# Kernel optimization log

Measured on AMD Instinct MI355X. Metric: run time of the kernel, lower is better.

## Reference

```python
import jax, jax.numpy as jnp
import numpy as np

N = 50000    # nodes
E = 640000   # edges (avg degree ~12.8)
IN_NF = 64   # raw atom features
D = 96       # hidden dim
H = 4 * D    # 384
L = 4        # RPETConv layers
G = 512      # graphs in the batch
NOUT = 2


def setup_inputs():
    key = jax.random.key(0)
    ks = iter(jax.random.split(key, 64))
    def lin(shape):
        fi = shape[-2]
        return jax.random.normal(next(ks), shape, jnp.float32) / np.float32(np.sqrt(fi))
    inp = {}
    inp['x'] = jax.random.normal(next(ks), (N, IN_NF), jnp.float32)
    inp['edge_attr'] = jax.random.normal(next(ks), (E, D), jnp.float32)
    inp['emb_W1'] = lin((IN_NF, H)); inp['emb_b1'] = jnp.zeros((H,), jnp.float32)
    inp['emb_W2'] = lin((H, D));     inp['emb_b2'] = jnp.zeros((D,), jnp.float32)
    for nm in ('Wq', 'Wk', 'Wv', 'ffn_W1', 'ffn_W2'):
        inp[nm] = lin((L, D, D))
    for nm in ('bq', 'bk', 'bv', 'ffn_b1', 'ffn_b2', 'n1_b', 'n2_b'):
        inp[nm] = jnp.zeros((L, D), jnp.float32)
    inp['n1_g'] = jnp.ones((L, D), jnp.float32)
    inp['n2_g'] = jnp.ones((L, D), jnp.float32)
    inp['u_W1'] = lin((D, H)); inp['u_b1'] = jnp.zeros((H,), jnp.float32)
    inp['u_W2'] = lin((H, H)); inp['u_b2'] = jnp.zeros((H,), jnp.float32)
    inp['u_g'] = jnp.ones((H,), jnp.float32); inp['u_b'] = jnp.zeros((H,), jnp.float32)
    inp['clf_W'] = lin((H, NOUT)); inp['clf_b'] = jnp.zeros((NOUT,), jnp.float32)
    inp['rec_W1'] = lin((H, H)); inp['rec_b1'] = jnp.zeros((H,), jnp.float32)
    inp['rec_W2'] = lin((H, IN_NF)); inp['rec_b2'] = jnp.zeros((IN_NF,), jnp.float32)
    inp['edge_index'] = jax.random.randint(next(ks), (2, E), 0, N, jnp.int32)
    inp['batch_index'] = jnp.sort(jax.random.randint(next(ks), (N,), 0, G, jnp.int32))
    return inp


def _ln(x, g, b):
    # torch.nn.LayerNorm, eps=1e-5
    m = x.mean(-1, keepdims=True)
    v = ((x - m) ** 2).mean(-1, keepdims=True)
    return (x - m) * jax.lax.rsqrt(v + 1e-5) * g + b


def _forward(fs, edge_index, batch_index):
    (x, edge_attr, emb_W1, emb_b1, emb_W2, emb_b2,
     Wq, bq, Wk, bk, Wv, bv, n1_g, n1_b,
     ffn_W1, ffn_b1, ffn_W2, ffn_b2, n2_g, n2_b,
     u_W1, u_b1, u_W2, u_b2, u_g, u_b,
     clf_W, clf_b, rec_W1, rec_b1, rec_W2, rec_b2) = fs
    src, dst = edge_index[0], edge_index[1]  # PyG: x_j = x[src], x_i = x[dst]
    scale = D ** -0.5
    # atom embedding MLP
    h = jax.nn.relu(x @ emb_W1 + emb_b1) @ emb_W2 + emb_b2  # [N, D]
    for l in range(L):
        x_i = h[dst]                  # [E, D] target gather
        px = h[src] + edge_attr       # [E, D] source + relative positional edge attr
        q = x_i @ Wq[l] + bq[l]
        k = px @ Wk[l] + bk[l]
        v = px @ Wv[l] + bv[l]
        ae = jnp.exp((q * k).sum(-1) * scale)  # [E] (original uses raw exp, no max-sub)
        # faithful quirk: softmax denominator segmented over SOURCE index
        s = ae / jax.ops.segment_sum(ae, src, num_segments=N)[src]
        # aggregation (aggr='add') goes to TARGET index
        agg = jax.ops.segment_sum(s[:, None] * v, dst, num_segments=N)  # [N, D]
        h1 = _ln(h + agg, n1_g[l], n1_b[l])
        f = jax.nn.elu(h1 @ ffn_W1[l] + ffn_b1[l]) @ ffn_W2[l] + ffn_b2[l]
        h = _ln(f + h1, n2_g[l], n2_b[l])
    # updim
    u = jax.nn.leaky_relu(h @ u_W1 + u_b1, 0.01) @ u_W2 + u_b2
    u = _ln(u, u_g, u_b)              # [N, H]
    # mean readout per graph
    cnt = jnp.maximum(jax.ops.segment_sum(jnp.ones((N,), u.dtype), batch_index, num_segments=G), 1.0)
    pooled = jax.ops.segment_sum(u, batch_index, num_segments=G) / cnt[:, None]  # [G, H]
    out = pooled @ clf_W + clf_b      # [G, NOUT]
    r = jax.nn.relu(u @ rec_W1 + rec_b1) @ rec_W2 + rec_b2  # [N, IN_NF]
    return (out, r)


def reference(x, edge_attr, emb_W1, emb_b1, emb_W2, emb_b2, Wq, bq, Wk, bk, Wv, bv, n1_g, n1_b, ffn_W1, ffn_b1, ffn_W2, ffn_b2, n2_g, n2_b, u_W1, u_b1, u_W2, u_b2, u_g, u_b, clf_W, clf_b, rec_W1, rec_b1, rec_W2, rec_b2, edge_index, batch_index):
    fs = (x, edge_attr, emb_W1, emb_b1, emb_W2, emb_b2, Wq, bq, Wk, bk, Wv, bv, n1_g, n1_b,
          ffn_W1, ffn_b1, ffn_W2, ffn_b2, n2_g, n2_b, u_W1, u_b1, u_W2, u_b2, u_g, u_b,
          clf_W, clf_b, rec_W1, rec_b1, rec_W2, rec_b2)
    return _forward(fs, edge_index, batch_index)
```

## Files before the change

### kernel.cpp

```cpp
#include <hip/hip_runtime.h>
#include <math.h>

#define N_NODES 50000
#define N_EDGES 640000
#define INF_ 64
#define DD 96
#define HH 384
#define NLAYERS 4
#define NGRAPH 512
#define NOUT_ 2
#define MAXDEG 64

#define ACT_NONE 0
#define ACT_RELU 1
#define ACT_ELU 2
#define ACT_LEAKY 3

typedef unsigned int uint;
typedef unsigned short ushort;
typedef __attribute__((ext_vector_type(8))) short v8s;
typedef __attribute__((ext_vector_type(4))) float v4f;

__device__ __forceinline__ float bf_lo(uint u) { return __uint_as_float(u << 16); }
__device__ __forceinline__ float bf_hi(uint u) { return __uint_as_float(u & 0xffff0000u); }
__device__ __forceinline__ float bfs(ushort s) { return __uint_as_float(((uint)s) << 16); }
__device__ __forceinline__ ushort f2bf(float f)
{
    uint u = __float_as_uint(f);
    return (ushort)((u + 0x7fffu + ((u >> 16) & 1u)) >> 16);
}

template<int BN, int ACT, bool ACCUM, bool OUT16>
__global__ __launch_bounds__(256)
void gemm_mf(const ushort* __restrict__ A, const ushort* __restrict__ Bt,
             const float* __restrict__ bias, float* __restrict__ C32,
             ushort* __restrict__ C16, int M, int Nc, int K)
{
    const int BM = 128, LDA = 40;
    const int FN = BN / 32;
    __shared__ ushort As[BM * LDA];
    __shared__ ushort Bs[BN * LDA];
    int tid = threadIdx.x;
    int lane = tid & 63, wave = tid >> 6;
    int ln15 = lane & 15, quad = lane >> 4;
    int wm = (wave >> 1) * 64, wn = (wave & 1) * (BN / 2);
    int bm0 = blockIdx.x * BM, bn0 = blockIdx.y * BN;

    v4f acc[4][FN];
    #pragma unroll
    for (int i = 0; i < 4; i++)
        #pragma unroll
        for (int j = 0; j < FN; j++) acc[i][j] = (v4f){0.f, 0.f, 0.f, 0.f};

    for (int k0 = 0; k0 < K; k0 += 32) {
        #pragma unroll
        for (int it = 0; it < 2; it++) {
            int u = it * 256 + tid;
            int r = u >> 2, c8 = (u & 3) * 8;
            int row = bm0 + r;
            int4 v = make_int4(0, 0, 0, 0);
            if (row < M) v = *(const int4*)&A[(size_t)row * K + k0 + c8];
            *(int4*)&As[r * LDA + c8] = v;
        }
        #pragma unroll
        for (int it = 0; it < (BN * 4 + 255) / 256; it++) {
            int u = it * 256 + tid;
            if ((BN * 4) % 256 == 0 || u < BN * 4) {
                int r = u >> 2, c8 = (u & 3) * 8;
                *(int4*)&Bs[r * LDA + c8] =
                    *(const int4*)&Bt[(size_t)(bn0 + r) * K + k0 + c8];
            }
        }
        __syncthreads();
        v8s af[4], bf[FN];
        #pragma unroll
        for (int i = 0; i < 4; i++)
            af[i] = *(const v8s*)&As[(wm + i * 16 + ln15) * LDA + quad * 8];
        #pragma unroll
        for (int j = 0; j < FN; j++)
            bf[j] = *(const v8s*)&Bs[(wn + j * 16 + ln15) * LDA + quad * 8];
        #pragma unroll
        for (int i = 0; i < 4; i++)
            #pragma unroll
            for (int j = 0; j < FN; j++)
                acc[i][j] = __builtin_amdgcn_mfma_f32_16x16x32_bf16(
                    af[i], bf[j], acc[i][j], 0, 0, 0);
        __syncthreads();
    }
    #pragma unroll
    for (int i = 0; i < 4; i++) {
        #pragma unroll
        for (int j = 0; j < FN; j++) {
            int col = bn0 + wn + j * 16 + ln15;
            float bsv = bias ? bias[col] : 0.f;
            #pragma unroll
            for (int r = 0; r < 4; r++) {
                int row = bm0 + wm + i * 16 + quad * 4 + r;
                if (row >= M) continue;
                float v = acc[i][j][r] + bsv;
                if (ACCUM) v += C32[(size_t)row * Nc + col];
                if (ACT == ACT_RELU)       v = fmaxf(v, 0.f);
                else if (ACT == ACT_ELU)   v = v > 0.f ? v : expm1f(v);
                else if (ACT == ACT_LEAKY) v = v > 0.f ? v : 0.01f * v;
                if (OUT16) C16[(size_t)row * Nc + col] = f2bf(v);
                else       C32[(size_t)row * Nc + col] = v;
            }
        }
    }
}

__device__ __forceinline__ float wave_reduce_sum(float v)
{
    #pragma unroll
    for (int o = 32; o > 0; o >>= 1) v += __shfl_xor(v, o, 64);
    return v;
}

__global__ __launch_bounds__(256)
void cvt16(const float* __restrict__ in, ushort* __restrict__ out, long n)
{
    long i = ((long)blockIdx.x * 256 + threadIdx.x) * 4;
    if (i >= n) return;
    float4 v = *(const float4*)&in[i];
    ushort4 o;
    o.x = f2bf(v.x); o.y = f2bf(v.y); o.z = f2bf(v.z); o.w = f2bf(v.w);
    *(ushort4*)&out[i] = o;
}

__global__ __launch_bounds__(256)
void wqk_k(const float* __restrict__ Wq, const float* __restrict__ Wk,
           const float* __restrict__ bq, float* __restrict__ Wcat, float* __restrict__ bcat)
{
    int l = blockIdx.y;
    int idx = blockIdx.x * 256 + threadIdx.x;
    const float* wq = Wq + (size_t)l * DD * DD;
    const float* wk = Wk + (size_t)l * DD * DD;
    if (idx < DD * DD) {
        int k = idx / DD, j = idx % DD;
        float s = 0.f;
        for (int t = 0; t < DD; t++) s += wq[k * DD + t] * wk[j * DD + t];
        Wcat[(size_t)l * DD * 4 * DD + (size_t)k * 4 * DD + 288 + j] = s;
    }
    if (idx < DD) {
        int j = idx;
        float s = 0.f;
        for (int t = 0; t < DD; t++) s += bq[l * DD + t] * wk[j * DD + t];
        bcat[l * 4 * DD + 288 + j] = s;
    }
}

__global__ __launch_bounds__(256)
void pack_k(const float* __restrict__ Wq, const float* __restrict__ Wk,
            const float* __restrict__ Wv, const float* __restrict__ bq,
            const float* __restrict__ bk, const float* __restrict__ bv,
            float* __restrict__ Wcat, float* __restrict__ bcat)
{
    int idx = blockIdx.x * 256 + threadIdx.x;
    if (idx >= NLAYERS * DD * 288) return;
    int l = idx / (DD * 288);
    int rem = idx % (DD * 288);
    int k = rem / 288, n = rem % 288;
    int which = n / DD, j = n % DD;
    const float* W = which == 0 ? Wq : (which == 1 ? Wk : Wv);
    Wcat[(size_t)l * DD * 4 * DD + (size_t)k * 4 * DD + n] =
        W[(size_t)l * DD * DD + k * DD + j];
    if (k == 0) {
        const float* bb = which == 0 ? bq : (which == 1 ? bk : bv);
        bcat[l * 4 * DD + n] = bb[l * DD + j];
    }
}

#define NPACK 22
struct PackArgs {
    const float* src[NPACK];
    ushort* dst[NPACK];
    int K[NPACK], N[NPACK];
};
__global__ __launch_bounds__(256)
void packT_k(PackArgs pa)
{
    int w = blockIdx.y;
    int K = pa.K[w], N = pa.N[w];
    int idx = blockIdx.x * 256 + threadIdx.x;
    if (idx >= K * N) return;
    int n = idx / K, k = idx % K;
    pa.dst[w][(size_t)n * K + k] = f2bf(pa.src[w][(size_t)k * N + n]);
}

__global__ __launch_bounds__(256)
void scatter_k(const int* __restrict__ src, const int* __restrict__ dst,
               int* __restrict__ deg, int2* __restrict__ pe)
{
    int e = blockIdx.x * 256 + threadIdx.x;
    if (e >= N_EDGES) return;
    int d = dst[e];
    int c = atomicAdd(&deg[d], 1);
    if (c < MAXDEG) pe[(size_t)d * MAXDEG + c] = make_int2(src[e], e);
}

template<bool EA16>
__global__ __launch_bounds__(256)
void edge1w(const ushort* __restrict__ qkv16, const void* __restrict__ eaP,
            const int2* __restrict__ pe, const int* __restrict__ deg,
            float* __restrict__ ae_slot, float* __restrict__ denom, float scale)
{
    int lane = threadIdx.x & 63;
    int half = lane >> 5, l32 = lane & 31;
    int d = blockIdx.x * 4 + (threadIdx.x >> 6);
    if (d >= N_NODES) return;
    int cnt = deg[d]; if (cnt > MAXDEG) cnt = MAXDEG;
    if (cnt == 0) return;
    const uint* qrow = (const uint*)(qkv16 + (size_t)d * 384);
    const uint* prow = (const uint*)(qkv16 + (size_t)d * 384 + 288);
    uint qu0 = qrow[l32], pu0 = prow[l32];
    uint qu1 = 0, pu1 = 0;
    if (l32 < 16) { qu1 = qrow[32 + l32]; pu1 = prow[32 + l32]; }
    float q00 = bf_lo(qu0), q01 = bf_hi(qu0), q10 = bf_lo(qu1), q11 = bf_hi(qu1);
    float p00 = bf_lo(pu0), p01 = bf_hi(pu0), p10 = bf_lo(pu1), p11 = bf_hi(pu1);
    int2 pr = pe[(size_t)d * MAXDEG + lane];
    for (int cb = 0; cb < cnt; cb += 4) {
        float dots[2];
        int sxu[2];
        #pragma unroll
        for (int u = 0; u < 2; u++) {
            int myc = cb + 2 * u + half;
            int cc = myc < cnt ? myc : cnt - 1;
            int sx = __shfl(pr.x, cc);
            int ex = __shfl(pr.y, cc);
            sxu[u] = sx;
            const uint* krow = (const uint*)(qkv16 + (size_t)sx * 384 + 96);
            uint ku0 = krow[l32];
            float e00, e01, e10 = 0.f, e11 = 0.f;
            uint ku1 = 0;
            if (EA16) {
                const uint* er = (const uint*)eaP + (size_t)ex * 48;
                uint eu0 = er[l32]; e00 = bf_lo(eu0); e01 = bf_hi(eu0);
                if (l32 < 16) {
                    uint eu1 = er[32 + l32]; e10 = bf_lo(eu1); e11 = bf_hi(eu1);
                    ku1 = krow[32 + l32];
                }
            } else {
                const float* er = (const float*)eaP + (size_t)ex * DD;
                float2 ef0 = *(const float2*)&er[2 * l32]; e00 = ef0.x; e01 = ef0.y;
                if (l32 < 16) {
                    float2 ef1 = *(const float2*)&er[64 + 2 * l32]; e10 = ef1.x; e11 = ef1.y;
                    ku1 = krow[32 + l32];
                }
            }
            float dot = q00 * bf_lo(ku0) + q01 * bf_hi(ku0)
                      + p00 * e00 + p01 * e01 + p10 * e10 + p11 * e11;
            if (l32 < 16) dot += q10 * bf_lo(ku1) + q11 * bf_hi(ku1);
            dots[u] = dot;
        }
        #pragma unroll
        for (int o = 16; o > 0; o >>= 1) {
            dots[0] += __shfl_xor(dots[0], o);
            dots[1] += __shfl_xor(dots[1], o);
        }
        #pragma unroll
        for (int u = 0; u < 2; u++) {
            int myc = cb + 2 * u + half;
            if (l32 == 0 && myc < cnt) {
                float v = __expf(dots[u] * scale);
                ae_slot[(size_t)d * MAXDEG + myc] = v;
                atomicAdd(&denom[sxu[u]], v);
            }
        }
    }
}

template<bool EA16>
__global__ __launch_bounds__(256)
void edge2w(const ushort* __restrict__ qkv16, const void* __restrict__ eaP,
            const float* __restrict__ ae_slot, const float* __restrict__ denom,
            const int2* __restrict__ pe, const int* __restrict__ deg,
            float* __restrict__ agg, ushort* __restrict__ T16)
{
    int lane = threadIdx.x & 63;
    int half = lane >> 5, l32 = lane & 31;
    int d = blockIdx.x * 4 + (threadIdx.x >> 6);
    if (d >= N_NODES) return;
    int cnt = deg[d]; if (cnt > MAXDEG) cnt = MAXDEG;
    int2 pr = pe[(size_t)d * MAXDEG + lane];
    float ar = ae_slot[(size_t)d * MAXDEG + lane];
    float a00 = 0.f, a01 = 0.f, a10 = 0.f, a11 = 0.f;
    float t00 = 0.f, t01 = 0.f, t10 = 0.f, t11 = 0.f;
    for (int cb = 0; cb < cnt; cb += 4) {
        #pragma unroll
        for (int u = 0; u < 2; u++) {
            int myc = cb + 2 * u + half;
            int cc = myc < cnt ? myc : cnt - 1;
            int sx = __shfl(pr.x, cc);
            int ex = __shfl(pr.y, cc);
            float ae = __shfl(ar, cc);
            float w = (myc < cnt) ? ae / denom[sx] : 0.f;
            const uint* vrow = (const uint*)(qkv16 + (size_t)sx * 384 + 192);
            uint vu0 = vrow[l32];
            float e00, e01, e10 = 0.f, e11 = 0.f;
            uint vu1 = 0;
            if (EA16) {
                const uint* er = (const uint*)eaP + (size_t)ex * 48;
                uint eu0 = er[l32]; e00 = bf_lo(eu0); e01 = bf_hi(eu0);
                if (l32 < 16) {
                    uint eu1 = er[32 + l32]; e10 = bf_lo(eu1); e11 = bf_hi(eu1);
                    vu1 = vrow[32 + l32];
                }
            } else {
                const float* er = (const float*)eaP + (size_t)ex * DD;
                float2 ef0 = *(const float2*)&er[2 * l32]; e00 = ef0.x; e01 = ef0.y;
                if (l32 < 16) {
                    float2 ef1 = *(const float2*)&er[64 + 2 * l32]; e10 = ef1.x; e11 = ef1.y;
                    vu1 = vrow[32 + l32];
                }
            }
            a00 += w * bf_lo(vu0); a01 += w * bf_hi(vu0);
            t00 += w * e00; t01 += w * e01;
            if (l32 < 16) {
                a10 += w * bf_lo(vu1); a11 += w * bf_hi(vu1);
                t10 += w * e10; t11 += w * e11;
            }
        }
    }
    a00 += __shfl_xor(a00, 32); a01 += __shfl_xor(a01, 32);
    a10 += __shfl_xor(a10, 32); a11 += __shfl_xor(a11, 32);
    t00 += __shfl_xor(t00, 32); t01 += __shfl_xor(t01, 32);
    t10 += __shfl_xor(t10, 32); t11 += __shfl_xor(t11, 32);
    if (half == 0) {
        *(float2*)&agg[(size_t)d * DD + 2 * l32] = make_float2(a00, a01);
        ((uint*)T16)[(size_t)d * 48 + l32] = ((uint)f2bf(t01) << 16) | f2bf(t00);
        if (l32 < 16) {
            *(float2*)&agg[(size_t)d * DD + 64 + 2 * l32] = make_float2(a10, a11);
            ((uint*)T16)[(size_t)d * 48 + 32 + l32] = ((uint)f2bf(t11) << 16) | f2bf(t10);
        }
    }
}

template<int RL, int BMODE>
__global__ __launch_bounds__(256)
void ln_b(const ushort* __restrict__ a, const void* __restrict__ bP,
          const float* __restrict__ g, const float* __restrict__ beta,
          ushort* __restrict__ out, int M)
{
    int wave = threadIdx.x >> 6;
    int lane = threadIdx.x & 63;
    int row = blockIdx.x * 4 + wave;
    if (row >= M) return;
    const int NE = (RL + 63) / 64;
    float vals[NE];
    float s = 0.f;
    #pragma unroll
    for (int i = 0; i < NE; i++) {
        int j = lane + i * 64;
        float x = 0.f;
        if (j < RL) {
            x = bfs(a[(size_t)row * RL + j]);
            if (BMODE == 1) x += ((const float*)bP)[(size_t)row * RL + j];
            if (BMODE == 2) x += bfs(((const ushort*)bP)[(size_t)row * RL + j]);
        }
        vals[i] = x; s += x;
    }
    s = wave_reduce_sum(s);
    float mean = s / RL;
    float sq = 0.f;
    #pragma unroll
    for (int i = 0; i < NE; i++) {
        int j = lane + i * 64;
        if (j < RL) { float dd = vals[i] - mean; sq += dd * dd; }
    }
    sq = wave_reduce_sum(sq);
    float rstd = rsqrtf(sq / RL + 1e-5f);
    #pragma unroll
    for (int i = 0; i < NE; i++) {
        int j = lane + i * 64;
        if (j < RL)
            out[(size_t)row * RL + j] = f2bf((vals[i] - mean) * rstd * g[j] + beta[j]);
    }
}

#define PCHUNK 64
__global__ __launch_bounds__(192)
void pool2_k(const ushort* __restrict__ u, const int* __restrict__ batch,
             float* __restrict__ pooled, float* __restrict__ cnt)
{
    int j = threadIdx.x;
    int n0 = blockIdx.x * PCHUNK;
    if (n0 >= N_NODES) return;
    int n1 = n0 + PCHUNK; if (n1 > N_NODES) n1 = N_NODES;
    float a0 = 0.f, a1 = 0.f;
    int cur = batch[n0];
    int runStart = n0;
    for (int n = n0; n < n1; n++) {
        int bg = batch[n];
        if (bg != cur) {
            atomicAdd(&pooled[(size_t)cur * HH + 2 * j], a0);
            atomicAdd(&pooled[(size_t)cur * HH + 2 * j + 1], a1);
            if (j == 0) atomicAdd(&cnt[cur], (float)(n - runStart));
            a0 = 0.f; a1 = 0.f; cur = bg; runStart = n;
        }
        uint v = ((const uint*)u)[(size_t)n * 192 + j];
        a0 += bf_lo(v); a1 += bf_hi(v);
    }
    atomicAdd(&pooled[(size_t)cur * HH + 2 * j], a0);
    atomicAdd(&pooled[(size_t)cur * HH + 2 * j + 1], a1);
    if (j == 0) atomicAdd(&cnt[cur], (float)(n1 - runStart));
}

__global__ __launch_bounds__(64)
void clf_k(const float* __restrict__ pooled, const float* __restrict__ cnt,
           const float* __restrict__ W, const float* __restrict__ bcl,
           float* __restrict__ out)
{
    int g = blockIdx.x;
    int lane = threadIdx.x;
    float c = cnt[g]; c = c > 1.f ? c : 1.f;
    float inv = 1.f / c;
    float a0 = 0.f, a1 = 0.f;
    #pragma unroll
    for (int i = 0; i < 6; i++) {
        int j = lane + i * 64;
        float pv = pooled[(size_t)g * HH + j] * inv;
        a0 += pv * W[j * 2 + 0];
        a1 += pv * W[j * 2 + 1];
    }
    a0 = wave_reduce_sum(a0);
    a1 = wave_reduce_sum(a1);
    if (lane == 0) {
        out[g * 2 + 0] = a0 + bcl[0];
        out[g * 2 + 1] = a1 + bcl[1];
    }
}

extern "C" void kernel_launch(void* const* d_in, const int* in_sizes, int n_in,
                              void* d_out, int out_size, void* d_ws, size_t ws_size,
                              hipStream_t stream)
{
    const float* x       = (const float*)d_in[0];
    const float* ea      = (const float*)d_in[1];
    const float* emb_W1  = (const float*)d_in[2];
    const float* emb_b1  = (const float*)d_in[3];
    const float* emb_W2  = (const float*)d_in[4];
    const float* emb_b2  = (const float*)d_in[5];
    const float* Wq      = (const float*)d_in[6];
    const float* Wk      = (const float*)d_in[7];
    const float* Wv      = (const float*)d_in[8];
    const float* ffn_W1  = (const float*)d_in[9];
    const float* ffn_W2  = (const float*)d_in[10];
    const float* bq      = (const float*)d_in[11];
    const float* bk      = (const float*)d_in[12];
    const float* bv      = (const float*)d_in[13];
    const float* ffn_b1  = (const float*)d_in[14];
    const float* ffn_b2  = (const float*)d_in[15];
    const float* n1_b    = (const float*)d_in[16];
    const float* n2_b    = (const float*)d_in[17];
    const float* n1_g    = (const float*)d_in[18];
    const float* n2_g    = (const float*)d_in[19];
    const float* u_W1    = (const float*)d_in[20];
    const float* u_b1    = (const float*)d_in[21];
    const float* u_W2    = (const float*)d_in[22];
    const float* u_b2    = (const float*)d_in[23];
    const float* u_g     = (const float*)d_in[24];
    const float* u_bb    = (const float*)d_in[25];
    const float* clf_W   = (const float*)d_in[26];
    const float* clf_b   = (const float*)d_in[27];
    const float* rec_W1  = (const float*)d_in[28];
    const float* rec_b1  = (const float*)d_in[29];
    const float* rec_W2  = (const float*)d_in[30];
    const float* rec_b2  = (const float*)d_in[31];
    const int* edge_index = (const int*)d_in[32];
    const int* batch     = (const int*)d_in[33];
    const int* srcI = edge_index;
    const int* dstI = edge_index + N_EDGES;

    float* out   = (float*)d_out;
    float* r_out = out + NGRAPH * NOUT_;

    char* base = (char*)d_ws;
    size_t off = 0;
    auto alloc = [&](size_t bytes) -> char* {
        char* r = base + off;
        off += (bytes + 255) & ~(size_t)255;
        return r;
    };
    ushort* h16     = (ushort*)alloc((size_t)N_NODES * DD * 2);
    ushort* qkv16   = (ushort*)alloc((size_t)N_NODES * HH * 2);
    float*  agg     = (float*) alloc((size_t)N_NODES * DD * 4);
    ushort* T16     = (ushort*)alloc((size_t)N_NODES * DD * 2);
    ushort* h116    = (ushort*)alloc((size_t)N_NODES * DD * 2);
    int2*   pe      = (int2*)  alloc((size_t)N_NODES * MAXDEG * 8);
    float*  ae_slot = (float*) alloc((size_t)N_NODES * MAXDEG * 4);
    ushort* f116    = (ushort*)alloc((size_t)N_NODES * DD * 2);
    float*  denom   = (float*) alloc((size_t)N_NODES * 4);
    int*    deg     = (int*)   alloc((size_t)N_NODES * 4);
    float*  pooled  = (float*) alloc((size_t)NGRAPH * HH * 4);
    float*  cnt     = (float*) alloc(NGRAPH * 4);
    float*  Wcat    = (float*) alloc((size_t)NLAYERS * DD * 4 * DD * 4);
    float*  bcat    = (float*) alloc((size_t)NLAYERS * 4 * DD * 4);
    ushort* x16     = (ushort*)alloc((size_t)N_NODES * INF_ * 2);
    ushort* embW1T  = (ushort*)alloc((size_t)HH * INF_ * 2);
    ushort* embW2T  = (ushort*)alloc((size_t)DD * HH * 2);
    ushort* WcatT   = (ushort*)alloc((size_t)NLAYERS * HH * DD * 2);
    ushort* WvT     = (ushort*)alloc((size_t)NLAYERS * DD * DD * 2);
    ushort* fW1T    = (ushort*)alloc((size_t)NLAYERS * DD * DD * 2);
    ushort* fW2T    = (ushort*)alloc((size_t)NLAYERS * DD * DD * 2);
    ushort* uW1T    = (ushort*)alloc((size_t)HH * DD * 2);
    ushort* uW2T    = (ushort*)alloc((size_t)HH * HH * 2);
    ushort* recW1T  = (ushort*)alloc((size_t)HH * HH * 2);
    ushort* recW2T  = (ushort*)alloc((size_t)INF_ * HH * 2);
    ushort* ea16 = (ushort*)alloc((size_t)N_EDGES * DD * 2);
    bool use_ea16 = (ws_size >= off);
    const void* eaP = use_ea16 ? (const void*)ea16 : (const void*)ea;

    ushort* t16    = qkv16;
    ushort* upre16 = (ushort*)agg;
    ushort* u16    = (ushort*)pe;
    ushort* rtmp16 = qkv16;

    dim3 blk(256);
    const int GB = (N_NODES + 127) / 128;
    const float scale = 1.f / sqrtf((float)DD);

    wqk_k<<<dim3(36, NLAYERS), blk, 0, stream>>>(Wq, Wk, bq, Wcat, bcat);
    pack_k<<<(NLAYERS * DD * 288 + 255) / 256, blk, 0, stream>>>(
        Wq, Wk, Wv, bq, bk, bv, Wcat, bcat);
    PackArgs pa;
    int pi = 0;
    auto addp = [&](const float* s, ushort* d, int K, int N) {
        pa.src[pi] = s; pa.dst[pi] = d; pa.K[pi] = K; pa.N[pi] = N; pi++;
    };
    addp(emb_W1, embW1T, INF_, HH);
    addp(emb_W2, embW2T, HH, DD);
    for (int l = 0; l < NLAYERS; l++) addp(Wcat + (size_t)l * DD * 4 * DD, WcatT + (size_t)l * HH * DD, DD, HH);
    for (int l = 0; l < NLAYERS; l++) addp(Wv + (size_t)l * DD * DD, WvT + (size_t)l * DD * DD, DD, DD);
    for (int l = 0; l < NLAYERS; l++) addp(ffn_W1 + (size_t)l * DD * DD, fW1T + (size_t)l * DD * DD, DD, DD);
    for (int l = 0; l < NLAYERS; l++) addp(ffn_W2 + (size_t)l * DD * DD, fW2T + (size_t)l * DD * DD, DD, DD);
    addp(u_W1, uW1T, DD, HH);
    addp(u_W2, uW2T, HH, HH);
    addp(rec_W1, recW1T, HH, HH);
    addp(rec_W2, recW2T, HH, INF_);
    packT_k<<<dim3(576, NPACK), blk, 0, stream>>>(pa);

    cvt16<<<((size_t)N_NODES * INF_ / 4 + 255) / 256, blk, 0, stream>>>(
        x, x16, (long)N_NODES * INF_);
    if (use_ea16)
        cvt16<<<((size_t)N_EDGES * DD / 4 + 255) / 256, blk, 0, stream>>>(
            ea, ea16, (long)N_EDGES * DD);

    gemm_mf<128, ACT_RELU, false, true><<<dim3(GB, 3), blk, 0, stream>>>(
        x16, embW1T, emb_b1, nullptr, t16, N_NODES, HH, INF_);
    gemm_mf<96, ACT_NONE, false, true><<<dim3(GB, 1), blk, 0, stream>>>(
        t16, embW2T, emb_b2, nullptr, h16, N_NODES, DD, HH);

    hipMemsetAsync(deg, 0, N_NODES * sizeof(int), stream);
    scatter_k<<<(N_EDGES + 255) / 256, blk, 0, stream>>>(srcI, dstI, deg, pe);

    const int EGRID = (N_NODES + 3) / 4;
    for (int l = 0; l < NLAYERS; l++) {
        gemm_mf<128, ACT_NONE, false, true><<<dim3(GB, 3), blk, 0, stream>>>(
            h16, WcatT + (size_t)l * HH * DD, bcat + (size_t)l * 4 * DD,
            nullptr, qkv16, N_NODES, HH, DD);

        hipMemsetAsync(denom, 0, N_NODES * sizeof(float), stream);
        if (use_ea16) {
            edge1w<true><<<EGRID, blk, 0, stream>>>(
                qkv16, eaP, pe, deg, ae_slot, denom, scale);
            edge2w<true><<<EGRID, blk, 0, stream>>>(
                qkv16, eaP, ae_slot, denom, pe, deg, agg, T16);
        } else {
            edge1w<false><<<EGRID, blk, 0, stream>>>(
                qkv16, eaP, pe, deg, ae_slot, denom, scale);
            edge2w<false><<<EGRID, blk, 0, stream>>>(
                qkv16, eaP, ae_slot, denom, pe, deg, agg, T16);
        }

        gemm_mf<96, ACT_NONE, true, false><<<dim3(GB, 1), blk, 0, stream>>>(
            T16, WvT + (size_t)l * DD * DD, nullptr, agg, nullptr, N_NODES, DD, DD);

        ln_b<DD, 1><<<(N_NODES + 3) / 4, blk, 0, stream>>>(
            h16, agg, n1_g + (size_t)l * DD, n1_b + (size_t)l * DD, h116, N_NODES);

        gemm_mf<96, ACT_ELU, false, true><<<dim3(GB, 1), blk, 0, stream>>>(
            h116, fW1T + (size_t)l * DD * DD, ffn_b1 + (size_t)l * DD,
            nullptr, f116, N_NODES, DD, DD);
        gemm_mf<96, ACT_NONE, false, true><<<dim3(GB, 1), blk, 0, stream>>>(
            f116, fW2T + (size_t)l * DD * DD, ffn_b2 + (size_t)l * DD,
            nullptr, T16, N_NODES, DD, DD);
        ln_b<DD, 2><<<(N_NODES + 3) / 4, blk, 0, stream>>>(
            T16, h116, n2_g + (size_t)l * DD, n2_b + (size_t)l * DD, h16, N_NODES);
    }

    gemm_mf<128, ACT_LEAKY, false, true><<<dim3(GB, 3), blk, 0, stream>>>(
        h16, uW1T, u_b1, nullptr, t16, N_NODES, HH, DD);
    gemm_mf<128, ACT_NONE, false, true><<<dim3(GB, 3), blk, 0, stream>>>(
        t16, uW2T, u_b2, nullptr, upre16, N_NODES, HH, HH);
    ln_b<HH, 0><<<(N_NODES + 3) / 4, blk, 0, stream>>>(
        upre16, nullptr, u_g, u_bb, u16, N_NODES);

    hipMemsetAsync(pooled, 0, (size_t)(NGRAPH * HH + NGRAPH) * sizeof(float), stream);
    pool2_k<<<(N_NODES + PCHUNK - 1) / PCHUNK, 192, 0, stream>>>(u16, batch, pooled, cnt);
    clf_k<<<NGRAPH, 64, 0, stream>>>(pooled, cnt, clf_W, clf_b, out);

    gemm_mf<128, ACT_RELU, false, true><<<dim3(GB, 3), blk, 0, stream>>>(
        u16, recW1T, rec_b1, nullptr, rtmp16, N_NODES, HH, HH);
    gemm_mf<64, ACT_NONE, false, false><<<dim3(GB, 1), blk, 0, stream>>>(
        rtmp16, recW2T, rec_b2, r_out, nullptr, N_NODES, INF_, HH);
}
```

Before: 1.662 ms.

## Fuse GEMM with residual LayerNorm and regroup edge kernels into 16-lane groups

```diff
diff --git a/kernel.cpp b/kernel.cpp
--- a/kernel.cpp
+++ b/kernel.cpp
@@ -109,6 +109,138 @@
     }
 }
 
+template<bool ACC32>
+__global__ __launch_bounds__(256)
+void gemm_ln(const ushort* __restrict__ A, const ushort* __restrict__ Bt,
+             const float* __restrict__ bias, const float* __restrict__ C32,
+             const ushort* __restrict__ add16,
+             const float* __restrict__ g, const float* __restrict__ beta,
+             ushort* __restrict__ out, int M, int K)
+{
+    const int BM = 128, LDA = 40, FN = 3;
+    __shared__ ushort As[BM * LDA];
+    __shared__ ushort Bs[96 * LDA];
+    __shared__ float2 red[2][2][64];
+    int tid = threadIdx.x;
+    int lane = tid & 63, wave = tid >> 6;
+    int ln15 = lane & 15, quad = lane >> 4;
+    int wm = (wave >> 1) * 64, wn = (wave & 1) * 48;
+    int bm0 = blockIdx.x * BM;
+
+    v4f acc[4][FN];
+    #pragma unroll
+    for (int i = 0; i < 4; i++)
+        #pragma unroll
+        for (int j = 0; j < FN; j++) acc[i][j] = (v4f){0.f, 0.f, 0.f, 0.f};
+
+    for (int k0 = 0; k0 < K; k0 += 32) {
+        #pragma unroll
+        for (int it = 0; it < 2; it++) {
+            int u = it * 256 + tid;
+            int r = u >> 2, c8 = (u & 3) * 8;
+            int row = bm0 + r;
+            int4 v = make_int4(0, 0, 0, 0);
+            if (row < M) v = *(const int4*)&A[(size_t)row * K + k0 + c8];
+            *(int4*)&As[r * LDA + c8] = v;
+        }
+        #pragma unroll
+        for (int it = 0; it < 2; it++) {
+            int u = it * 256 + tid;
+            if (u < 384) {
+                int r = u >> 2, c8 = (u & 3) * 8;
+                *(int4*)&Bs[r * LDA + c8] =
+                    *(const int4*)&Bt[(size_t)r * K + k0 + c8];
+            }
+        }
+        __syncthreads();
+        v8s af[4], bf[FN];
+        #pragma unroll
+        for (int i = 0; i < 4; i++)
+            af[i] = *(const v8s*)&As[(wm + i * 16 + ln15) * LDA + quad * 8];
+        #pragma unroll
+        for (int j = 0; j < FN; j++)
+            bf[j] = *(const v8s*)&Bs[(wn + j * 16 + ln15) * LDA + quad * 8];
+        #pragma unroll
+        for (int i = 0; i < 4; i++)
+            #pragma unroll
+            for (int j = 0; j < FN; j++)
+                acc[i][j] = __builtin_amdgcn_mfma_f32_16x16x32_bf16(
+                    af[i], bf[j], acc[i][j], 0, 0, 0);
+        __syncthreads();
+    }
+
+    float s1a[4][4], s2a[4][4];
+    #pragma unroll
+    for (int i = 0; i < 4; i++)
+        #pragma unroll
+        for (int r = 0; r < 4; r++) { s1a[i][r] = 0.f; s2a[i][r] = 0.f; }
+
+    #pragma unroll
+    for (int i = 0; i < 4; i++) {
+        #pragma unroll
+        for (int j = 0; j < FN; j++) {
+            int col = wn + j * 16 + ln15;
+            float bsv = bias ? bias[col] : 0.f;
+            #pragma unroll
+            for (int r = 0; r < 4; r++) {
+                int row = bm0 + wm + i * 16 + quad * 4 + r;
+                float v = acc[i][j][r] + bsv;
+                if (row < M) {
+                    if (ACC32) v += C32[(size_t)row * DD + col];
+                    v += bfs(add16[(size_t)row * DD + col]);
+                }
+                acc[i][j][r] = v;
+                s1a[i][r] += v; s2a[i][r] += v * v;
+            }
+        }
+    }
+    #pragma unroll
+    for (int o = 1; o <= 8; o <<= 1) {
+        #pragma unroll
+        for (int i = 0; i < 4; i++)
+            #pragma unroll
+            for (int r = 0; r < 4; r++) {
+                s1a[i][r] += __shfl_xor(s1a[i][r], o);
+                s2a[i][r] += __shfl_xor(s2a[i][r], o);
+            }
+    }
+    if (ln15 == 0) {
+        #pragma unroll
+        for (int i = 0; i < 4; i++)
+            #pragma unroll
+            for (int r = 0; r < 4; r++)
+                red[wave >> 1][wave & 1][i * 16 + quad * 4 + r] =
+                    make_float2(s1a[i][r], s2a[i][r]);
+    }
+    __syncthreads();
+    float gj[FN], bj[FN];
+    #pragma unroll
+    for (int j = 0; j < FN; j++) {
+        gj[j] = g[wn + j * 16 + ln15];
+        bj[j] = beta[wn + j * 16 + ln15];
+    }
+    #pragma unroll
+    for (int i = 0; i < 4; i++) {
+        #pragma unroll
+        for (int r = 0; r < 4; r++) {
+            int row = bm0 + wm + i * 16 + quad * 4 + r;
+            if (row >= M) continue;
+            float2 o = red[wave >> 1][(wave & 1) ^ 1][i * 16 + quad * 4 + r];
+            float tot1 = s1a[i][r] + o.x;
+            float tot2 = s2a[i][r] + o.y;
+            float mean = tot1 * (1.f / 96.f);
+            float var  = tot2 * (1.f / 96.f) - mean * mean;
+            float rstd = rsqrtf(var + 1e-5f);
+            #pragma unroll
+            for (int j = 0; j < FN; j++) {
+                int col = wn + j * 16 + ln15;
+                out[(size_t)row * DD + col] =
+                    f2bf((acc[i][j][r] - mean) * rstd * gj[j] + bj[j]);
+            }
+        }
+    }
+}
+
 __device__ __forceinline__ float wave_reduce_sum(float v)
 {
     #pragma unroll
@@ -205,62 +337,61 @@
             float* __restrict__ ae_slot, float* __restrict__ denom, float scale)
 {
     int lane = threadIdx.x & 63;
-    int half = lane >> 5, l32 = lane & 31;
+    int grp = lane >> 4, t = lane & 15;
     int d = blockIdx.x * 4 + (threadIdx.x >> 6);
     if (d >= N_NODES) return;
     int cnt = deg[d]; if (cnt > MAXDEG) cnt = MAXDEG;
     if (cnt == 0) return;
-    const uint* qrow = (const uint*)(qkv16 + (size_t)d * 384);
-    const uint* prow = (const uint*)(qkv16 + (size_t)d * 384 + 288);
-    uint qu0 = qrow[l32], pu0 = prow[l32];
-    uint qu1 = 0, pu1 = 0;
-    if (l32 < 16) { qu1 = qrow[32 + l32]; pu1 = prow[32 + l32]; }
-    float q00 = bf_lo(qu0), q01 = bf_hi(qu0), q10 = bf_lo(qu1), q11 = bf_hi(qu1);
-    float p00 = bf_lo(pu0), p01 = bf_hi(pu0), p10 = bf_lo(pu1), p11 = bf_hi(pu1);
+    const uint* row = (const uint*)qkv16 + (size_t)d * 192;
+    uint qa = row[t], qb = row[16 + t], qc = row[32 + t];
+    uint pa = row[144 + t], pb = row[160 + t], pc = row[176 + t];
+    float q0l = bf_lo(qa), q0h = bf_hi(qa), q1l = bf_lo(qb), q1h = bf_hi(qb),
+          q2l = bf_lo(qc), q2h = bf_hi(qc);
+    float p0l = bf_lo(pa), p0h = bf_hi(pa), p1l = bf_lo(pb), p1h = bf_hi(pb),
+          p2l = bf_lo(pc), p2h = bf_hi(pc);
     int2 pr = pe[(size_t)d * MAXDEG + lane];
-    for (int cb = 0; cb < cnt; cb += 4) {
+    for (int cb = 0; cb < cnt; cb += 8) {
         float dots[2];
         int sxu[2];
         #pragma unroll
         for (int u = 0; u < 2; u++) {
-            int myc = cb + 2 * u + half;
+            int myc = cb + u * 4 + grp;
             int cc = myc < cnt ? myc : cnt - 1;
             int sx = __shfl(pr.x, cc);
             int ex = __shfl(pr.y, cc);
             sxu[u] = sx;
-            const uint* krow = (const uint*)(qkv16 + (size_t)sx * 384 + 96);
-            uint ku0 = krow[l32];
-            float e00, e01, e10 = 0.f, e11 = 0.f;
-            uint ku1 = 0;
+            const uint* kr = (const uint*)qkv16 + (size_t)sx * 192 + 48;
+            uint k0 = kr[t], k1 = kr[16 + t], k2 = kr[32 + t];
+            float e0l, e0h, e1l, e1h, e2l, e2h;
             if (EA16) {
                 const uint* er = (const uint*)eaP + (size_t)ex * 48;
-                uint eu0 = er[l32]; e00 = bf_lo(eu0); e01 = bf_hi(eu0);
-                if (l32 < 16) {
-                    uint eu1 = er[32 + l32]; e10 = bf_lo(eu1); e11 = bf_hi(eu1);
-                    ku1 = krow[32 + l32];
-                }
+                uint e0 = er[t], e1 = er[16 + t], e2 = er[32 + t];
+                e0l = bf_lo(e0); e0h = bf_hi(e0);
+                e1l = bf_lo(e1); e1h = bf_hi(e1);
+                e2l = bf_lo(e2); e2h = bf_hi(e2);
             } else {
                 const float* er = (const float*)eaP + (size_t)ex * DD;
-                float2 ef0 = *(const float2*)&er[2 * l32]; e00 = ef0.x; e01 = ef0.y;
-                if (l32 < 16) {
-                    float2 ef1 = *(const float2*)&er[64 + 2 * l32]; e10 = ef1.x; e11 = ef1.y;
-                    ku1 = krow[32 + l32];
-                }
-            }
-            float dot = q00 * bf_lo(ku0) + q01 * bf_hi(ku0)
-                      + p00 * e00 + p01 * e01 + p10 * e10 + p11 * e11;
-            if (l32 < 16) dot += q10 * bf_lo(ku1) + q11 * bf_hi(ku1);
-            dots[u] = dot;
-        }
-        #pragma unroll
-        for (int o = 16; o > 0; o >>= 1) {
+                float2 f0 = *(const float2*)&er[2 * t];
+                float2 f1 = *(const float2*)&er[32 + 2 * t];
+                float2 f2 = *(const float2*)&er[64 + 2 * t];
+                e0l = f0.x; e0h = f0.y; e1l = f1.x; e1h = f1.y;
+                e2l = f2.x; e2h = f2.y;
+            }
+            dots[u] = q0l * bf_lo(k0) + q0h * bf_hi(k0)
+                    + q1l * bf_lo(k1) + q1h * bf_hi(k1)
+                    + q2l * bf_lo(k2) + q2h * bf_hi(k2)
+                    + p0l * e0l + p0h * e0h + p1l * e1l + p1h * e1h
+                    + p2l * e2l + p2h * e2h;
+        }
+        #pragma unroll
+        for (int o = 8; o > 0; o >>= 1) {
             dots[0] += __shfl_xor(dots[0], o);
             dots[1] += __shfl_xor(dots[1], o);
         }
         #pragma unroll
         for (int u = 0; u < 2; u++) {
-            int myc = cb + 2 * u + half;
-            if (l32 == 0 && myc < cnt) {
+            int myc = cb + u * 4 + grp;
+            if (t == 0 && myc < cnt) {
                 float v = __expf(dots[u] * scale);
                 ae_slot[(size_t)d * MAXDEG + myc] = v;
                 atomicAdd(&denom[sxu[u]], v);
@@ -277,61 +408,65 @@
             float* __restrict__ agg, ushort* __restrict__ T16)
 {
     int lane = threadIdx.x & 63;
-    int half = lane >> 5, l32 = lane & 31;
+    int grp = lane >> 4, t = lane & 15;
     int d = blockIdx.x * 4 + (threadIdx.x >> 6);
     if (d >= N_NODES) return;
     int cnt = deg[d]; if (cnt > MAXDEG) cnt = MAXDEG;
     int2 pr = pe[(size_t)d * MAXDEG + lane];
     float ar = ae_slot[(size_t)d * MAXDEG + lane];
-    float a00 = 0.f, a01 = 0.f, a10 = 0.f, a11 = 0.f;
-    float t00 = 0.f, t01 = 0.f, t10 = 0.f, t11 = 0.f;
-    for (int cb = 0; cb < cnt; cb += 4) {
+    float a0l = 0.f, a0h = 0.f, a1l = 0.f, a1h = 0.f, a2l = 0.f, a2h = 0.f;
+    float t0l = 0.f, t0h = 0.f, t1l = 0.f, t1h = 0.f, t2l = 0.f, t2h = 0.f;
+    for (int cb = 0; cb < cnt; cb += 8) {
         #pragma unroll
         for (int u = 0; u < 2; u++) {
-            int myc = cb + 2 * u + half;
+            int myc = cb + u * 4 + grp;
             int cc = myc < cnt ? myc : cnt - 1;
             int sx = __shfl(pr.x, cc);
             int ex = __shfl(pr.y, cc);
             float ae = __shfl(ar, cc);
             float w = (myc < cnt) ? ae / denom[sx] : 0.f;
-            const uint* vrow = (const uint*)(qkv16 + (size_t)sx * 384 + 192);
-            uint vu0 = vrow[l32];
-            float e00, e01, e10 = 0.f, e11 = 0.f;
-            uint vu1 = 0;
+            const uint* vr = (const uint*)qkv16 + (size_t)sx * 192 + 96;
+            uint v0 = vr[t], v1 = vr[16 + t], v2 = vr[32 + t];
+            float e0l, e0h, e1l, e1h, e2l, e2h;
             if (EA16) {
                 const uint* er = (const uint*)eaP + (size_t)ex * 48;
-                uint eu0 = er[l32]; e00 = bf_lo(eu0); e01 = bf_hi(eu0);
-                if (l32 < 16) {
-                    uint eu1 = er[32 + l32]; e10 = bf_lo(eu1); e11 = bf_hi(eu1);
-                    vu1 = vrow[32 + l32];
-                }
+                uint e0 = er[t], e1 = er[16 + t], e2 = er[32 + t];
+                e0l = bf_lo(e0); e0h = bf_hi(e0);
+                e1l = bf_lo(e1); e1h = bf_hi(e1);
+                e2l = bf_lo(e2); e2h = bf_hi(e2);
             } else {
                 const float* er = (const float*)eaP + (size_t)ex * DD;
-                float2 ef0 = *(const float2*)&er[2 * l32]; e00 = ef0.x; e01 = ef0.y;
-                if (l32 < 16) {
-                    float2 ef1 = *(const float2*)&er[64 + 2 * l32]; e10 = ef1.x; e11 = ef1.y;
-                    vu1 = vrow[32 + l32];
-                }
-            }
-            a00 += w * bf_lo(vu0); a01 += w * bf_hi(vu0);
-            t00 += w * e00; t01 += w * e01;
-            if (l32 < 16) {
-                a10 += w * bf_lo(vu1); a11 += w * bf_hi(vu1);
-                t10 += w * e10; t11 += w * e11;
-            }
-        }
-    }
-    a00 += __shfl_xor(a00, 32); a01 += __shfl_xor(a01, 32);
-    a10 += __shfl_xor(a10, 32); a11 += __shfl_xor(a11, 32);
-    t00 += __shfl_xor(t00, 32); t01 += __shfl_xor(t01, 32);
-    t10 += __shfl_xor(t10, 32); t11 += __shfl_xor(t11, 32);
-    if (half == 0) {
-        *(float2*)&agg[(size_t)d * DD + 2 * l32] = make_float2(a00, a01);
-        ((uint*)T16)[(size_t)d * 48 + l32] = ((uint)f2bf(t01) << 16) | f2bf(t00);
-        if (l32 < 16) {
-            *(float2*)&agg[(size_t)d * DD + 64 + 2 * l32] = make_float2(a10, a11);
-            ((uint*)T16)[(size_t)d * 48 + 32 + l32] = ((uint)f2bf(t11) << 16) | f2bf(t10);
-        }
+                float2 f0 = *(const float2*)&er[2 * t];
+                float2 f1 = *(const float2*)&er[32 + 2 * t];
+                float2 f2 = *(const float2*)&er[64 + 2 * t];
+                e0l = f0.x; e0h = f0.y; e1l = f1.x; e1h = f1.y;
+                e2l = f2.x; e2h = f2.y;
+            }
+            a0l += w * bf_lo(v0); a0h += w * bf_hi(v0);
+            a1l += w * bf_lo(v1); a1h += w * bf_hi(v1);
+            a2l += w * bf_lo(v2); a2h += w * bf_hi(v2);
+            t0l += w * e0l; t0h += w * e0h;
+            t1l += w * e1l; t1h += w * e1h;
+            t2l += w * e2l; t2h += w * e2h;
+        }
+    }
+    #pragma unroll
+    for (int o = 16; o <= 32; o <<= 1) {
+        a0l += __shfl_xor(a0l, o); a0h += __shfl_xor(a0h, o);
+        a1l += __shfl_xor(a1l, o); a1h += __shfl_xor(a1h, o);
+        a2l += __shfl_xor(a2l, o); a2h += __shfl_xor(a2h, o);
+        t0l += __shfl_xor(t0l, o); t0h += __shfl_xor(t0h, o);
+        t1l += __shfl_xor(t1l, o); t1h += __shfl_xor(t1h, o);
+        t2l += __shfl_xor(t2l, o); t2h += __shfl_xor(t2h, o);
+    }
+    if (grp == 0) {
+        *(float2*)&agg[(size_t)d * DD + 2 * t]      = make_float2(a0l, a0h);
+        *(float2*)&agg[(size_t)d * DD + 32 + 2 * t] = make_float2(a1l, a1h);
+        *(float2*)&agg[(size_t)d * DD + 64 + 2 * t] = make_float2(a2l, a2h);
+        uint* Tw = (uint*)T16 + (size_t)d * 48;
+        Tw[t]      = ((uint)f2bf(t0h) << 16) | f2bf(t0l);
+        Tw[16 + t] = ((uint)f2bf(t1h) << 16) | f2bf(t1l);
+        Tw[32 + t] = ((uint)f2bf(t2h) << 16) | f2bf(t2l);
     }
 }
 
@@ -572,20 +707,18 @@
                 qkv16, eaP, ae_slot, denom, pe, deg, agg, T16);
         }
 
-        gemm_mf<96, ACT_NONE, true, false><<<dim3(GB, 1), blk, 0, stream>>>(
-            T16, WvT + (size_t)l * DD * DD, nullptr, agg, nullptr, N_NODES, DD, DD);
-
-        ln_b<DD, 1><<<(N_NODES + 3) / 4, blk, 0, stream>>>(
-            h16, agg, n1_g + (size_t)l * DD, n1_b + (size_t)l * DD, h116, N_NODES);
+        gemm_ln<true><<<GB, blk, 0, stream>>>(
+            T16, WvT + (size_t)l * DD * DD, nullptr, agg, h16,
+            n1_g + (size_t)l * DD, n1_b + (size_t)l * DD, h116, N_NODES, DD);
 
         gemm_mf<96, ACT_ELU, false, true><<<dim3(GB, 1), blk, 0, stream>>>(
             h116, fW1T + (size_t)l * DD * DD, ffn_b1 + (size_t)l * DD,
             nullptr, f116, N_NODES, DD, DD);
-        gemm_mf<96, ACT_NONE, false, true><<<dim3(GB, 1), blk, 0, stream>>>(
+
+        gemm_ln<false><<<GB, blk, 0, stream>>>(
             f116, fW2T + (size_t)l * DD * DD, ffn_b2 + (size_t)l * DD,
-            nullptr, T16, N_NODES, DD, DD);
-        ln_b<DD, 2><<<(N_NODES + 3) / 4, blk, 0, stream>>>(
-            T16, h116, n2_g + (size_t)l * DD, n2_b + (size_t)l * DD, h16, N_NODES);
+            nullptr, h116, n2_g + (size_t)l * DD, n2_b + (size_t)l * DD,
+            h16, N_NODES, DD);
     }
 
     gemm_mf<128, ACT_LEAKY, false, true><<<dim3(GB, 3), blk, 0, stream>>>(
```

Measured after the change: 1.556 ms. 6.3% less time.
